# Performance work log

Hardware: AMD Instinct MI355X
Metric: run time of the kernel (lower is better)

The kernel has to match this reference:

```python
import jax, jax.numpy as jnp
import numpy as np
from jax import lax

D_MODEL, D_STATE, D_CONV, EXPAND = 1024, 16, 4, 2
D_INNER = D_MODEL * EXPAND
LN_EPS = 1e-5


def _silu(v):
    return v * jax.nn.sigmoid(v)


def setup_inputs() -> dict:
    key = jax.random.key(0)
    ks = jax.random.split(key, 12)
    B, T = 4, 2048
    x = jax.random.normal(ks[0], (B, T, D_MODEL), dtype=jnp.float32)
    W_in = jax.random.normal(ks[1], (2 * D_INNER, D_MODEL), dtype=jnp.float32) * (D_MODEL ** -0.5)
    conv_w = jax.random.normal(ks[2], (D_INNER, 1, D_CONV), dtype=jnp.float32) * (D_CONV ** -0.5)
    conv_b = jax.random.normal(ks[3], (D_INNER,), dtype=jnp.float32) * 0.01
    W_x = jax.random.normal(ks[4], (2 * D_STATE, D_INNER), dtype=jnp.float32) * (D_INNER ** -0.5)
    dt_init_std = D_INNER ** -0.5
    W_dt = jax.random.uniform(ks[5], (D_INNER, D_INNER), minval=-dt_init_std, maxval=dt_init_std, dtype=jnp.float32)
    # bias = inverse softplus of dt sampled log-uniform in [dt_min, dt_max]
    dt = jnp.exp(jax.random.uniform(ks[6], (D_INNER,)) * (np.log(0.1) - np.log(0.001)) + np.log(0.001))
    b_dt = dt + jnp.log(-jnp.expm1(-dt))
    A_log = jnp.log(jnp.arange(1, D_STATE + 1, dtype=jnp.float32) * 0.5)
    D_param = jnp.ones((D_INNER,), dtype=jnp.float32)
    W_out = jax.random.normal(ks[7], (D_MODEL, D_INNER), dtype=jnp.float32) * (D_MODEL ** -0.5)
    ln_g = jnp.ones((D_INNER,), dtype=jnp.float32)
    ln_b = jnp.zeros((D_INNER,), dtype=jnp.float32)
    return {"x": x, "W_in": W_in, "conv_w": conv_w, "conv_b": conv_b, "W_x": W_x,
            "W_dt": W_dt, "b_dt": b_dt, "A_log": A_log, "D_param": D_param,
            "W_out": W_out, "ln_g": ln_g, "ln_b": ln_b}


def _forward(x, W_in, conv_w, conv_b, W_x, W_dt, b_dt, A_log, D_param, W_out, ln_g, ln_b):
    B, T, _ = x.shape
    xz = jnp.einsum('btd,ed->bte', x, W_in)            # (B,T,2*d_inner)
    xp, z = xz[..., :D_INNER], xz[..., D_INNER:]
    # depthwise causal conv1d (left pad d_conv-1, keep first T outputs)
    xc = lax.conv_general_dilated(
        jnp.transpose(xp, (0, 2, 1)), conv_w,
        window_strides=(1,), padding=[(D_CONV - 1, 0)],
        feature_group_count=D_INNER,
        dimension_numbers=('NCH', 'OIH', 'NCH')) + conv_b[None, :, None]
    xc = _silu(jnp.transpose(xc, (0, 2, 1)))           # (B,T,d_inner)
    ssm = jnp.einsum('bti,si->bts', xc, W_x)           # (B,T,2*d_state)
    Bp, Cp = ssm[..., :D_STATE], ssm[..., D_STATE:]
    dt = jax.nn.softplus(jnp.einsum('bti,oi->bto', xc, W_dt) + b_dt)
    A = -jnp.exp(A_log)                                # (d_state,)

    def step(h, inp):
        x_t, b_t, c_t, dt_t = inp                      # (B,d),(B,s),(B,s),(B,d)
        dA = jnp.exp(dt_t[..., None] * A)              # (B,d_inner,d_state)
        h = dA * h + (dt_t[..., None] * b_t[:, None, :]) * x_t[..., None]
        y_t = jnp.einsum('bds,bs->bd', h, c_t)
        return h, y_t

    h0 = jnp.zeros((B, D_INNER, D_STATE), dtype=x.dtype)
    tm = lambda a: jnp.moveaxis(a, 1, 0)               # time-major
    _, ys = lax.scan(step, h0, (tm(xc), tm(Bp), tm(Cp), tm(dt)))
    y = jnp.moveaxis(ys, 0, 1)                         # (B,T,d_inner)

    mu = jnp.mean(y, axis=-1, keepdims=True)
    var = jnp.mean((y - mu) ** 2, axis=-1, keepdims=True)
    y = (y - mu) * lax.rsqrt(var + LN_EPS) * ln_g + ln_b
    y = y + xc * D_param
    y = y * _silu(z)
    return jnp.einsum('bti,di->btd', y, W_out)         # dropout is identity (eval)


def reference(x, W_in, conv_w, conv_b, W_x, W_dt, b_dt, A_log, D_param, W_out, ln_g, ln_b):
    return _forward(x, W_in, conv_w, conv_b, W_x, W_dt, b_dt, A_log, D_param, W_out, ln_g, ln_b)
```

## Files before the change

kernel.cpp:

```cpp
#include <hip/hip_runtime.h>
#include <hip/hip_bf16.h>
#include <math.h>
#include <stdint.h>

#define B_SZ 4
#define T_SZ 2048
#define DM   1024
#define DI   2048
#define DS   16
#define BT   (B_SZ*T_SZ)
#define NC   2176

typedef __attribute__((ext_vector_type(8))) short short8;
typedef __attribute__((ext_vector_type(4))) float f32x4;

__device__ __forceinline__ float siluf(float v) { return v / (1.f + __expf(-v)); }
__device__ __forceinline__ float softplusf(float x) {
    return fmaxf(x, 0.f) + log1pf(__expf(-fabsf(x)));
}
__device__ __forceinline__ unsigned short f2b(float f) {
    __hip_bfloat16 h = __float2bfloat16(f);
    return *reinterpret_cast<unsigned short*>(&h);
}
__device__ __forceinline__ float b2f(unsigned short u) {
    unsigned v = (unsigned)u << 16;
    float f;
    __builtin_memcpy(&f, &v, 4);
    return f;
}
__device__ __forceinline__ void gld_lds16(const void* g, void* l) {
    __builtin_amdgcn_global_load_lds(
        (const __attribute__((address_space(1))) unsigned int*)g,
        (__attribute__((address_space(3))) unsigned int*)l,
        16, 0, 0);
}

__global__ __launch_bounds__(256)
void cvt_bf16(const float* __restrict__ src, unsigned short* __restrict__ dst, int n4)
{
    int i = blockIdx.x * 256 + threadIdx.x;
    if (i >= n4) return;
    float4 v = ((const float4*)src)[i];
    ushort4 o;
    o.x = f2b(v.x); o.y = f2b(v.y); o.z = f2b(v.z); o.w = f2b(v.w);
    ((ushort4*)dst)[i] = o;
}

__global__ __launch_bounds__(256)
void cvt_wc(const float* __restrict__ Wdt, const float* __restrict__ Wx,
            unsigned short* __restrict__ dst)
{
    const int n4 = NC * (DI / 4);
    int i = blockIdx.x * 256 + threadIdx.x;
    if (i >= n4) return;
    int row = i >> 9;
    int c4  = i & 511;
    float4 v;
    if (row < 2048)      v = ((const float4*)Wdt)[(size_t)row * 512 + c4];
    else if (row < 2080) v = ((const float4*)Wx)[(size_t)(row - 2048) * 512 + c4];
    else                 v = make_float4(0.f, 0.f, 0.f, 0.f);
    ushort4 o;
    o.x = f2b(v.x); o.y = f2b(v.y); o.z = f2b(v.z); o.w = f2b(v.w);
    ((ushort4*)dst)[i] = o;
}

__global__ __launch_bounds__(512)
void gemm_mfma(const unsigned short* __restrict__ A,
               const unsigned short* __restrict__ Bm,
               int M, int N, int K, int mode,
               const float* __restrict__ bias,
               void* __restrict__ o0, void* __restrict__ o1, void* __restrict__ o2)
{
    __shared__ unsigned short As[2][128 * 64];
    __shared__ unsigned short Bs[2][128 * 64];

    const int npn = N >> 7;
    const int pid = blockIdx.x;
    const int gsz = 16 * npn;
    const int gid = pid / gsz;
    const int pm  = gid * 16 + (pid % 16);
    const int pn  = (pid % gsz) / 16;
    const int bm  = pm * 128;
    const int bn  = pn * 128;

    const int tid  = threadIdx.x;
    const int lane = tid & 63;
    const int wave = tid >> 6;
    const int wm   = (wave >> 2) * 64;
    const int wn   = (wave & 3) * 32;

    f32x4 zero4 = {0.f, 0.f, 0.f, 0.f};
    f32x4 acc[4][2];
#pragma unroll
    for (int i = 0; i < 4; i++)
#pragma unroll
        for (int j = 0; j < 2; j++) acc[i][j] = zero4;

    const int sr    = tid >> 3;
    const int sgran = (tid & 7) ^ ((tid >> 3) & 7);
    const unsigned short* Ag = A  + (size_t)(bm + sr) * K + sgran * 8;
    const unsigned short* Bg = Bm + (size_t)(bn + sr) * K + sgran * 8;
    const size_t rowK64 = (size_t)64 * K;

    const int fr = lane & 15;
    const int fg = lane >> 4;
    int aoff[4][2], boff[2][2];
#pragma unroll
    for (int i = 0; i < 4; i++)
#pragma unroll
        for (int kk = 0; kk < 2; kk++) {
            const int l = (wm + i * 16 + fr) * 128 + (fg + 4 * kk) * 16;
            aoff[i][kk] = l ^ (((l >> 7) & 7) << 4);
        }
#pragma unroll
    for (int j = 0; j < 2; j++)
#pragma unroll
        for (int kk = 0; kk < 2; kk++) {
            const int l = (wn + j * 16 + fr) * 128 + (fg + 4 * kk) * 16;
            boff[j][kk] = l ^ (((l >> 7) & 7) << 4);
        }

    gld_lds16(Ag,          &As[0][tid * 8]);
    gld_lds16(Ag + rowK64, &As[0][4096 + tid * 8]);
    gld_lds16(Bg,          &Bs[0][tid * 8]);
    gld_lds16(Bg + rowK64, &Bs[0][4096 + tid * 8]);
    __syncthreads();

    int cur = 0;
    for (int k0 = 0; k0 < K; k0 += 64) {
        if (k0 + 64 < K) {
            const size_t kn = (size_t)(k0 + 64);
            gld_lds16(Ag + kn,          &As[cur ^ 1][tid * 8]);
            gld_lds16(Ag + rowK64 + kn, &As[cur ^ 1][4096 + tid * 8]);
            gld_lds16(Bg + kn,          &Bs[cur ^ 1][tid * 8]);
            gld_lds16(Bg + rowK64 + kn, &Bs[cur ^ 1][4096 + tid * 8]);
        }
        const char* Ab = (const char*)&As[cur][0];
        const char* Bb = (const char*)&Bs[cur][0];
#pragma unroll
        for (int kk = 0; kk < 2; kk++) {
            short8 af[4], bf[2];
#pragma unroll
            for (int i = 0; i < 4; i++)
                af[i] = *(const short8*)(Ab + aoff[i][kk]);
#pragma unroll
            for (int j = 0; j < 2; j++)
                bf[j] = *(const short8*)(Bb + boff[j][kk]);
#pragma unroll
            for (int i = 0; i < 4; i++)
#pragma unroll
                for (int j = 0; j < 2; j++)
                    acc[i][j] = __builtin_amdgcn_mfma_f32_16x16x32_bf16(
                        af[i], bf[j], acc[i][j], 0, 0, 0);
        }
        __syncthreads();
        cur ^= 1;
    }

    const int cr0 = bm + wm + fg * 4;
    const int cc0 = bn + wn + fr;
#pragma unroll
    for (int i = 0; i < 4; i++) {
#pragma unroll
        for (int j = 0; j < 2; j++) {
            const int col = cc0 + j * 16;
#pragma unroll
            for (int r = 0; r < 4; r++) {
                const int row = cr0 + i * 16 + r;
                float v = acc[i][j][r];
                if (mode == 0) {
                    if (col < 2048)
                        ((unsigned short*)o0)[(size_t)row * 2048 + col] = f2b(v);
                    else
                        ((unsigned short*)o1)[(size_t)row * 2048 + col - 2048] = f2b(v);
                } else if (mode == 1) {
                    if (col < 2048) {
                        ((float*)o0)[(size_t)row * 2048 + col] = softplusf(v + bias[col]);
                    } else if (col < 2064) {
                        ((float*)o1)[(size_t)row * DS + (col - 2048)] = v;
                    } else if (col < 2080) {
                        ((float*)o2)[(size_t)row * DS + (col - 2064)] = v;
                    }
                } else {
                    ((float*)o0)[(size_t)row * N + col] = v;
                }
            }
        }
    }
}

__global__ __launch_bounds__(256)
void conv_silu(const unsigned short* __restrict__ xpb, const float* __restrict__ cw,
               const float* __restrict__ cb, unsigned short* __restrict__ xcb)
{
    const int bt  = blockIdx.x;
    const int t   = bt & (T_SZ - 1);
    const int i0  = threadIdx.x * 8;

    float acc[8];
    {
        float4 c0 = ((const float4*)cb)[threadIdx.x * 2];
        float4 c1 = ((const float4*)cb)[threadIdx.x * 2 + 1];
        acc[0]=c0.x; acc[1]=c0.y; acc[2]=c0.z; acc[3]=c0.w;
        acc[4]=c1.x; acc[5]=c1.y; acc[6]=c1.z; acc[7]=c1.w;
    }
    float4 w[8];
#pragma unroll
    for (int c = 0; c < 8; c++) w[c] = ((const float4*)cw)[i0 + c];

#pragma unroll
    for (int k = 0; k < 4; k++) {
        const int tt = t - 3 + k;
        if (tt >= 0) {
            short8 xv = *(const short8*)(xpb + (size_t)(bt - 3 + k) * DI + i0);
            const float* wk = (const float*)&w[0];
#pragma unroll
            for (int c = 0; c < 8; c++)
                acc[c] = fmaf(b2f((unsigned short)xv[c]), ((const float*)&w[c])[k], acc[c]);
            (void)wk;
        }
    }
    short8 o;
#pragma unroll
    for (int c = 0; c < 8; c++) o[c] = (short)f2b(siluf(acc[c]));
    *(short8*)(xcb + (size_t)bt * DI + i0) = o;
}

#define CH 16
#define CL (T_SZ / CH)

__global__ __launch_bounds__(256)
void scan2(const unsigned short* __restrict__ xcb, float* __restrict__ dty,
           const float* __restrict__ Bp, const float* __restrict__ Cp,
           const float* __restrict__ A_log)
{
    __shared__ float shH[CH][16][DS];
    __shared__ float shP[CH][16][DS];
    __shared__ float shI[CH][16][DS];
    const int tid = threadIdx.x;
    const int c = tid >> 4;
    const int g = tid & 15;
    const int b = blockIdx.y;
    const int d = blockIdx.x * 16 + g;

    float A[DS];
#pragma unroll
    for (int s = 0; s < DS; s++) A[s] = -__expf(A_log[s]);

    const size_t colbase = (size_t)b * T_SZ * DI + d;
    const unsigned short* xp = xcb + colbase + (size_t)c * CL * DI;
    float* dp = dty + colbase + (size_t)c * CL * DI;
    const float4* Bb = (const float4*)(Bp + ((size_t)b * T_SZ + c * CL) * DS);
    const float4* Cb = (const float4*)(Cp + ((size_t)b * T_SZ + c * CL) * DS);

    float h[DS], P[DS];
#pragma unroll
    for (int s = 0; s < DS; s++) { h[s] = 0.f; P[s] = 1.f; }

    for (int i = 0; i < CL; i++) {
        const float xv = b2f(xp[(size_t)i * DI]);
        const float dv = dp[(size_t)i * DI];
        float4 Bv[4] = {Bb[i*4+0], Bb[i*4+1], Bb[i*4+2], Bb[i*4+3]};
        const float* bs = (const float*)&Bv[0];
        const float dx = dv * xv;
#pragma unroll
        for (int s = 0; s < DS; s++) {
            const float dA = __expf(dv * A[s]);
            h[s] = fmaf(dA, h[s], dx * bs[s]);
            P[s] *= dA;
        }
    }
#pragma unroll
    for (int s = 0; s < DS; s += 4) {
        *(float4*)&shH[c][g][s] = make_float4(h[s], h[s+1], h[s+2], h[s+3]);
        *(float4*)&shP[c][g][s] = make_float4(P[s], P[s+1], P[s+2], P[s+3]);
    }
    __syncthreads();

    {
        const int g2 = tid >> 4, s2 = tid & 15;
        float hin = 0.f;
        shI[0][g2][s2] = 0.f;
        for (int cc = 1; cc < CH; cc++) {
            hin = fmaf(shP[cc-1][g2][s2], hin, shH[cc-1][g2][s2]);
            shI[cc][g2][s2] = hin;
        }
    }
    __syncthreads();

#pragma unroll
    for (int s = 0; s < DS; s++) h[s] = shI[c][g][s];
    for (int i = 0; i < CL; i++) {
        const float xv = b2f(xp[(size_t)i * DI]);
        const float dv = dp[(size_t)i * DI];
        float4 Bv[4] = {Bb[i*4+0], Bb[i*4+1], Bb[i*4+2], Bb[i*4+3]};
        float4 Cv[4] = {Cb[i*4+0], Cb[i*4+1], Cb[i*4+2], Cb[i*4+3]};
        const float* bs = (const float*)&Bv[0];
        const float* cs = (const float*)&Cv[0];
        const float dx = dv * xv;
        float yv = 0.f;
#pragma unroll
        for (int s = 0; s < DS; s++) {
            const float dA = __expf(dv * A[s]);
            h[s] = fmaf(dA, h[s], dx * bs[s]);
            yv = fmaf(h[s], cs[s], yv);
        }
        dp[(size_t)i * DI] = yv;
    }
}

__global__ __launch_bounds__(256)
void ln_fuse(const float* __restrict__ y, const unsigned short* __restrict__ xcb,
             const unsigned short* __restrict__ zb, const float* __restrict__ g,
             const float* __restrict__ bln, const float* __restrict__ Dp,
             unsigned short* __restrict__ yb)
{
    __shared__ float rs[256], rss[256];
    const int bt  = blockIdx.x;
    const int tid = threadIdx.x;
    const float* yr = y + (size_t)bt * DI;
    const unsigned short* xr = xcb + (size_t)bt * DI;
    const unsigned short* zr = zb + (size_t)bt * DI;
    unsigned short* orow = yb + (size_t)bt * DI;

    float v[8];
    float s = 0.f, ss = 0.f;
#pragma unroll
    for (int j = 0; j < 8; j++) {
        v[j] = yr[tid + j * 256];
        s  += v[j];
        ss += v[j] * v[j];
    }
    rs[tid] = s; rss[tid] = ss;
    __syncthreads();
    for (int off = 128; off > 0; off >>= 1) {
        if (tid < off) { rs[tid] += rs[tid + off]; rss[tid] += rss[tid + off]; }
        __syncthreads();
    }
    const float mu   = rs[0] * (1.f / DI);
    const float var  = rss[0] * (1.f / DI) - mu * mu;
    const float rstd = rsqrtf(var + 1e-5f);
#pragma unroll
    for (int j = 0; j < 8; j++) {
        const int dcol = tid + j * 256;
        float yn = (v[j] - mu) * rstd * g[dcol] + bln[dcol];
        yn += b2f(xr[dcol]) * Dp[dcol];
        yn *= siluf(b2f(zr[dcol]));
        orow[dcol] = f2b(yn);
    }
}

extern "C" void kernel_launch(void* const* d_in, const int* in_sizes, int n_in,
                              void* d_out, int out_size, void* d_ws, size_t ws_size,
                              hipStream_t stream)
{
    const float* x      = (const float*)d_in[0];
    const float* W_in   = (const float*)d_in[1];
    const float* conv_w = (const float*)d_in[2];
    const float* conv_b = (const float*)d_in[3];
    const float* W_x    = (const float*)d_in[4];
    const float* W_dt   = (const float*)d_in[5];
    const float* b_dt   = (const float*)d_in[6];
    const float* A_log  = (const float*)d_in[7];
    const float* D_par  = (const float*)d_in[8];
    const float* W_out  = (const float*)d_in[9];
    const float* ln_g   = (const float*)d_in[10];
    const float* ln_b   = (const float*)d_in[11];
    float* out = (float*)d_out;

    char* w = (char*)d_ws;
    const size_t MB = 1ull << 20;
    unsigned short* xpb    = (unsigned short*)(w);
    unsigned short* zb     = (unsigned short*)(w + 32 * MB);
    unsigned short* xcb    = (unsigned short*)(w + 64 * MB);
    float*          dts    = (float*)(w + 96 * MB);
    unsigned short* xb     = (unsigned short*)(w + 96 * MB);
    unsigned short* W_inb  = (unsigned short*)(w + 112 * MB);
    unsigned short* Wcb    = (unsigned short*)(w + 160 * MB);
    unsigned short* W_outb = (unsigned short*)(w + 169 * MB);
    float*          BpF    = (float*)(w + 174 * MB);
    float*          CpF    = BpF + (size_t)BT * DS;
    unsigned short* yb     = xpb;

    dim3 blk(256);
    dim3 blk512(512);

    cvt_bf16<<<dim3((BT * DM / 4 + 255) / 256), blk, 0, stream>>>(x, xb, BT * DM / 4);
    cvt_bf16<<<dim3((2 * DI * DM / 4 + 255) / 256), blk, 0, stream>>>(W_in, W_inb, 2 * DI * DM / 4);
    cvt_wc<<<dim3((NC * DI / 4 + 255) / 256), blk, 0, stream>>>(W_dt, W_x, Wcb);
    cvt_bf16<<<dim3((DM * DI / 4 + 255) / 256), blk, 0, stream>>>(W_out, W_outb, DM * DI / 4);

    gemm_mfma<<<dim3((BT / 128) * (2 * DI / 128)), blk512, 0, stream>>>(
        xb, W_inb, BT, 2 * DI, DM, 0, nullptr, xpb, zb, nullptr);

    conv_silu<<<dim3(BT), blk, 0, stream>>>(xpb, conv_w, conv_b, xcb);

    gemm_mfma<<<dim3((BT / 128) * (NC / 128)), blk512, 0, stream>>>(
        xcb, Wcb, BT, NC, DI, 1, b_dt, dts, BpF, CpF);

    scan2<<<dim3(DI / 16, B_SZ), blk, 0, stream>>>(xcb, dts, BpF, CpF, A_log);

    ln_fuse<<<dim3(BT), blk, 0, stream>>>(dts, xcb, zb, ln_g, ln_b, D_par, yb);

    gemm_mfma<<<dim3((BT / 128) * (DM / 128)), blk512, 0, stream>>>(
        yb, W_outb, BT, DM, DI, 2, nullptr, out, nullptr, nullptr);
}
```

Before: 644.1 us.

## Use 256x128 GEMM tiles with K=32 stages, XCD remap, and cheaper scan decay

The GEMM block tile changes from 128x128 to 256x128 with K-step 32, and each wave now computes a 64x64 subtile, so fragment reuse per LDS read goes up. Workgroup IDs are remapped across the 8 XCDs, and s_setprio is raised around the MFMA burst. In the scan, the per-state running product of decays is replaced by one sum of dt per chunk followed by exp(sum*A), which removes a multiply per state per step. The trade-offs are fewer workgroups per GEMM (some wave quantization risk), more accumulator registers, and twice as many K iterations and barriers.

```diff
diff --git a/kernel.cpp b/kernel.cpp
--- a/kernel.cpp
+++ b/kernel.cpp
@@ -71,98 +71,98 @@
                const float* __restrict__ bias,
                void* __restrict__ o0, void* __restrict__ o1, void* __restrict__ o2)
 {
-    __shared__ unsigned short As[2][128 * 64];
-    __shared__ unsigned short Bs[2][128 * 64];
-
+    __shared__ unsigned short As[2][256 * 32];
+    __shared__ unsigned short Bs[2][128 * 32];
+
+    const int npm = M >> 8;
     const int npn = N >> 7;
-    const int pid = blockIdx.x;
+    const int nwg = npm * npn;
+    const int q    = nwg >> 3;
+    const int pid  = (blockIdx.x & 7) * q + (blockIdx.x >> 3);
     const int gsz = 16 * npn;
     const int gid = pid / gsz;
     const int pm  = gid * 16 + (pid % 16);
     const int pn  = (pid % gsz) / 16;
-    const int bm  = pm * 128;
+    const int bm  = pm * 256;
     const int bn  = pn * 128;
 
     const int tid  = threadIdx.x;
     const int lane = tid & 63;
     const int wave = tid >> 6;
-    const int wm   = (wave >> 2) * 64;
-    const int wn   = (wave & 3) * 32;
+    const int wm   = (wave >> 1) * 64;
+    const int wn   = (wave & 1) * 64;
 
     f32x4 zero4 = {0.f, 0.f, 0.f, 0.f};
-    f32x4 acc[4][2];
+    f32x4 acc[4][4];
 #pragma unroll
     for (int i = 0; i < 4; i++)
 #pragma unroll
-        for (int j = 0; j < 2; j++) acc[i][j] = zero4;
-
-    const int sr    = tid >> 3;
-    const int sgran = (tid & 7) ^ ((tid >> 3) & 7);
+        for (int j = 0; j < 4; j++) acc[i][j] = zero4;
+
+    const int sr    = tid >> 2;
+    const int sgran = (tid & 3) ^ ((tid >> 3) & 3);
     const unsigned short* Ag = A  + (size_t)(bm + sr) * K + sgran * 8;
     const unsigned short* Bg = Bm + (size_t)(bn + sr) * K + sgran * 8;
-    const size_t rowK64 = (size_t)64 * K;
+    const size_t rowK128 = (size_t)128 * K;
 
     const int fr = lane & 15;
     const int fg = lane >> 4;
-    int aoff[4][2], boff[2][2];
-#pragma unroll
-    for (int i = 0; i < 4; i++)
-#pragma unroll
-        for (int kk = 0; kk < 2; kk++) {
-            const int l = (wm + i * 16 + fr) * 128 + (fg + 4 * kk) * 16;
-            aoff[i][kk] = l ^ (((l >> 7) & 7) << 4);
-        }
-#pragma unroll
-    for (int j = 0; j < 2; j++)
-#pragma unroll
-        for (int kk = 0; kk < 2; kk++) {
-            const int l = (wn + j * 16 + fr) * 128 + (fg + 4 * kk) * 16;
-            boff[j][kk] = l ^ (((l >> 7) & 7) << 4);
-        }
-
-    gld_lds16(Ag,          &As[0][tid * 8]);
-    gld_lds16(Ag + rowK64, &As[0][4096 + tid * 8]);
-    gld_lds16(Bg,          &Bs[0][tid * 8]);
-    gld_lds16(Bg + rowK64, &Bs[0][4096 + tid * 8]);
+    int aoff[4], boff[4];
+#pragma unroll
+    for (int i = 0; i < 4; i++) {
+        const int l = (wm + i * 16 + fr) * 64 + fg * 16;
+        aoff[i] = l ^ (((l >> 7) & 3) << 4);
+    }
+#pragma unroll
+    for (int j = 0; j < 4; j++) {
+        const int l = (wn + j * 16 + fr) * 64 + fg * 16;
+        boff[j] = l ^ (((l >> 7) & 3) << 4);
+    }
+
+#define STAGE(buf, kbase) do {                                        \
+        const size_t kb_ = (size_t)(kbase);                           \
+        gld_lds16(Ag + kb_,           &As[(buf)][tid * 8]);           \
+        gld_lds16(Ag + rowK128 + kb_, &As[(buf)][4096 + tid * 8]);    \
+        gld_lds16(Bg + kb_,           &Bs[(buf)][tid * 8]);           \
+    } while (0)
+
+    STAGE(0, 0);
     __syncthreads();
 
     int cur = 0;
-    for (int k0 = 0; k0 < K; k0 += 64) {
-        if (k0 + 64 < K) {
-            const size_t kn = (size_t)(k0 + 64);
-            gld_lds16(Ag + kn,          &As[cur ^ 1][tid * 8]);
-            gld_lds16(Ag + rowK64 + kn, &As[cur ^ 1][4096 + tid * 8]);
-            gld_lds16(Bg + kn,          &Bs[cur ^ 1][tid * 8]);
-            gld_lds16(Bg + rowK64 + kn, &Bs[cur ^ 1][4096 + tid * 8]);
-        }
+    for (int k0 = 0; k0 < K; k0 += 32) {
+        if (k0 + 32 < K) STAGE(cur ^ 1, k0 + 32);
+
         const char* Ab = (const char*)&As[cur][0];
         const char* Bb = (const char*)&Bs[cur][0];
-#pragma unroll
-        for (int kk = 0; kk < 2; kk++) {
-            short8 af[4], bf[2];
-#pragma unroll
-            for (int i = 0; i < 4; i++)
-                af[i] = *(const short8*)(Ab + aoff[i][kk]);
-#pragma unroll
-            for (int j = 0; j < 2; j++)
-                bf[j] = *(const short8*)(Bb + boff[j][kk]);
-#pragma unroll
-            for (int i = 0; i < 4; i++)
-#pragma unroll
-                for (int j = 0; j < 2; j++)
-                    acc[i][j] = __builtin_amdgcn_mfma_f32_16x16x32_bf16(
-                        af[i], bf[j], acc[i][j], 0, 0, 0);
-        }
+        short8 af[4], bf[4];
+#pragma unroll
+        for (int i = 0; i < 4; i++)
+            af[i] = *(const short8*)(Ab + aoff[i]);
+#pragma unroll
+        for (int j = 0; j < 4; j++)
+            bf[j] = *(const short8*)(Bb + boff[j]);
+
+        __builtin_amdgcn_s_setprio(1);
+#pragma unroll
+        for (int i = 0; i < 4; i++)
+#pragma unroll
+            for (int j = 0; j < 4; j++)
+                acc[i][j] = __builtin_amdgcn_mfma_f32_16x16x32_bf16(
+                    af[i], bf[j], acc[i][j], 0, 0, 0);
+        __builtin_amdgcn_s_setprio(0);
+
         __syncthreads();
         cur ^= 1;
     }
+#undef STAGE
 
     const int cr0 = bm + wm + fg * 4;
     const int cc0 = bn + wn + fr;
 #pragma unroll
     for (int i = 0; i < 4; i++) {
 #pragma unroll
-        for (int j = 0; j < 2; j++) {
+        for (int j = 0; j < 4; j++) {
             const int col = cc0 + j * 16;
 #pragma unroll
             for (int r = 0; r < 4; r++) {
@@ -213,11 +213,9 @@
         const int tt = t - 3 + k;
         if (tt >= 0) {
             short8 xv = *(const short8*)(xpb + (size_t)(bt - 3 + k) * DI + i0);
-            const float* wk = (const float*)&w[0];
 #pragma unroll
             for (int c = 0; c < 8; c++)
                 acc[c] = fmaf(b2f((unsigned short)xv[c]), ((const float*)&w[c])[k], acc[c]);
-            (void)wk;
         }
     }
     short8 o;
@@ -253,9 +251,10 @@
     const float4* Bb = (const float4*)(Bp + ((size_t)b * T_SZ + c * CL) * DS);
     const float4* Cb = (const float4*)(Cp + ((size_t)b * T_SZ + c * CL) * DS);
 
-    float h[DS], P[DS];
-#pragma unroll
-    for (int s = 0; s < DS; s++) { h[s] = 0.f; P[s] = 1.f; }
+    float h[DS];
+    float sdv = 0.f;
+#pragma unroll
+    for (int s = 0; s < DS; s++) h[s] = 0.f;
 
     for (int i = 0; i < CL; i++) {
         const float xv = b2f(xp[(size_t)i * DI]);
@@ -263,17 +262,20 @@
         float4 Bv[4] = {Bb[i*4+0], Bb[i*4+1], Bb[i*4+2], Bb[i*4+3]};
         const float* bs = (const float*)&Bv[0];
         const float dx = dv * xv;
+        sdv += dv;
 #pragma unroll
         for (int s = 0; s < DS; s++) {
             const float dA = __expf(dv * A[s]);
             h[s] = fmaf(dA, h[s], dx * bs[s]);
-            P[s] *= dA;
         }
     }
 #pragma unroll
     for (int s = 0; s < DS; s += 4) {
         *(float4*)&shH[c][g][s] = make_float4(h[s], h[s+1], h[s+2], h[s+3]);
-        *(float4*)&shP[c][g][s] = make_float4(P[s], P[s+1], P[s+2], P[s+3]);
+        *(float4*)&shP[c][g][s] = make_float4(__expf(sdv * A[s]),
+                                              __expf(sdv * A[s+1]),
+                                              __expf(sdv * A[s+2]),
+                                              __expf(sdv * A[s+3]));
     }
     __syncthreads();
 
@@ -390,18 +392,18 @@
     cvt_wc<<<dim3((NC * DI / 4 + 255) / 256), blk, 0, stream>>>(W_dt, W_x, Wcb);
     cvt_bf16<<<dim3((DM * DI / 4 + 255) / 256), blk, 0, stream>>>(W_out, W_outb, DM * DI / 4);
 
-    gemm_mfma<<<dim3((BT / 128) * (2 * DI / 128)), blk512, 0, stream>>>(
+    gemm_mfma<<<dim3((BT / 256) * (2 * DI / 128)), blk512, 0, stream>>>(
         xb, W_inb, BT, 2 * DI, DM, 0, nullptr, xpb, zb, nullptr);
 
     conv_silu<<<dim3(BT), blk, 0, stream>>>(xpb, conv_w, conv_b, xcb);
 
-    gemm_mfma<<<dim3((BT / 128) * (NC / 128)), blk512, 0, stream>>>(
+    gemm_mfma<<<dim3((BT / 256) * (NC / 128)), blk512, 0, stream>>>(
         xcb, Wcb, BT, NC, DI, 1, b_dt, dts, BpF, CpF);
 
     scan2<<<dim3(DI / 16, B_SZ), blk, 0, stream>>>(xcb, dts, BpF, CpF, A_log);
 
     ln_fuse<<<dim3(BT), blk, 0, stream>>>(dts, xcb, zb, ln_g, ln_b, D_par, yb);
 
-    gemm_mfma<<<dim3((BT / 128) * (DM / 128)), blk512, 0, stream>>>(
+    gemm_mfma<<<dim3((BT / 256) * (DM / 128)), blk512, 0, stream>>>(
         yb, W_outb, BT, DM, DI, 2, nullptr, out, nullptr, nullptr);
 }
```

Result: slower. 701.5 us (+8.9%).
